# Performance work log

Measured on AMD Instinct MI355X. Metric: run time of the kernel, lower is better.

Reference implementation:

```python
import jax, jax.numpy as jnp
import numpy as np

B, S, H = 2, 2048, 2048
NH, NG = 16, 4           # attention heads, query groups
HD = H // NH             # head_dim = 128
HPG = NH // NG           # heads per group = 4


def setup_inputs() -> dict:
    key = jax.random.key(0)
    ks = jax.random.split(key, 8)
    s = 0.02
    return {
        "hidden_states": jax.random.normal(ks[0], (B, S, H), dtype=jnp.float32),
        "attention_mask": jnp.ones((B, S), dtype=jnp.int32),
        "Wq": jax.random.normal(ks[1], (H, H), dtype=jnp.float32) * s,
        "bq": jnp.zeros((H,), dtype=jnp.float32),
        "Wk": jax.random.normal(ks[2], (HD * NG, H), dtype=jnp.float32) * s,
        "bk": jnp.zeros((HD * NG,), dtype=jnp.float32),
        "Wv": jax.random.normal(ks[3], (HD * NG, H), dtype=jnp.float32) * s,
        "bv": jnp.zeros((HD * NG,), dtype=jnp.float32),
    }


def reference(hidden_states, attention_mask, Wq, bq, Wk, bk, Wv, bv):
    b, s, _ = hidden_states.shape
    scale = 1.0 / np.sqrt(HD).astype(np.float32)
    # projections (torch Linear: x @ W.T + b)
    q = hidden_states @ Wq.T + bq                      # [b,s,H]
    k = hidden_states @ Wk.T + bk                      # [b,s,NG*HD]
    v = hidden_states @ Wv.T + bv
    # q grouped so that repeat_interleave of k/v along heads == broadcast over heads_per_group
    q = q.reshape(b, s, NG, HPG, HD)                   # heads = group-major order
    k = k.reshape(b, s, NG, HD)
    v = v.reshape(b, s, NG, HD)
    scores = jnp.einsum("bsgpd,btgd->bgpst", q, k) * scale  # [b,NG,HPG,s,s]
    # mask: positions with attention_mask == 0 get finfo.min added
    mask_add = jnp.where(attention_mask == 0,
                         jnp.finfo(scores.dtype).min,
                         jnp.float32(0.0))             # [b,t]
    scores = scores + mask_add[:, None, None, None, :]
    attn = jax.nn.softmax(scores, axis=-1)             # dropout is identity in eval
    out = jnp.einsum("bgpst,btgd->bsgpd", attn, v)     # [b,s,NG,HPG,HD]
    return out.reshape(b, s, NH * HD)
```

## Files before the change

### kernel.cpp

```cpp
#include <hip/hip_runtime.h>
#include <hip/hip_bf16.h>

#define B_ 2
#define S_ 2048
#define H_ 2048
#define NH_ 16
#define NG_ 4
#define HD_ 128
#define HPG_ 4

typedef __attribute__((ext_vector_type(8))) short short8;
typedef __attribute__((ext_vector_type(4))) short short4v;
typedef __attribute__((ext_vector_type(4))) float float4v;

#define MFMA_BF16 __builtin_amdgcn_mfma_f32_16x16x32_bf16

#if __has_builtin(__builtin_amdgcn_exp2f)
#define EXP2(x) __builtin_amdgcn_exp2f(x)
#else
#define EXP2(x) exp2f(x)
#endif

__device__ __forceinline__ void gload16(const void* g, void* l) {
    __builtin_amdgcn_global_load_lds(
        (const __attribute__((address_space(1))) unsigned int*)g,
        (__attribute__((address_space(3))) unsigned int*)l, 16, 0, 0);
}

__device__ __forceinline__ short bf16bits(float f) {
    union { __hip_bfloat16 h; short s; } u;
    u.h = __float2bfloat16(f);
    return u.s;
}

__global__ __launch_bounds__(256) void cvt_all(const float* __restrict__ hs,
                                               const float* __restrict__ wq,
                                               const float* __restrict__ wk,
                                               const float* __restrict__ wv,
                                               const int* __restrict__ mask,
                                               const float* __restrict__ bq,
                                               const float* __restrict__ bk,
                                               const float* __restrict__ bv,
                                               __hip_bfloat16* __restrict__ o_hs,
                                               __hip_bfloat16* __restrict__ o_wq,
                                               __hip_bfloat16* __restrict__ o_wk,
                                               __hip_bfloat16* __restrict__ o_wv,
                                               float* __restrict__ o_m,
                                               float* __restrict__ o_bc) {
    int i = blockIdx.x * 256 + threadIdx.x;
    if (blockIdx.x == 0) {
#pragma unroll
        for (int j = 0; j < 16; ++j) {
            int idx = threadIdx.x * 16 + j;
            o_m[idx] = mask[idx] ? 0.0f : -3.0e38f;
        }
    }
    if (blockIdx.x == 1) {
#pragma unroll
        for (int j = 0; j < 12; ++j) {
            int idx = j * 256 + threadIdx.x;
            float v = (idx < 2048) ? bq[idx] : (idx < 2560) ? bk[idx - 2048] : bv[idx - 2560];
            o_bc[idx] = v;
        }
    }
    const float* src;
    __hip_bfloat16* dst;
    int off;
    if (i < 1048576)      { src = hs; dst = o_hs; off = i; }
    else if (i < 1572864) { src = wq; dst = o_wq; off = i - 1048576; }
    else if (i < 1703936) { src = wk; dst = o_wk; off = i - 1572864; }
    else                  { src = wv; dst = o_wv; off = i - 1703936; }
    const float4* s4 = (const float4*)src;
    float4 a = s4[2 * (size_t)off];
    float4 b = s4[2 * (size_t)off + 1];
    union { short8 s; __hip_bfloat16 h[8]; } u;
    u.h[0] = __float2bfloat16(a.x); u.h[1] = __float2bfloat16(a.y);
    u.h[2] = __float2bfloat16(a.z); u.h[3] = __float2bfloat16(a.w);
    u.h[4] = __float2bfloat16(b.x); u.h[5] = __float2bfloat16(b.y);
    u.h[6] = __float2bfloat16(b.z); u.h[7] = __float2bfloat16(b.w);
    *(short8*)(dst + 8 * (size_t)off) = u.s;
}

__global__ __launch_bounds__(512, 2) void gemm_qkv3(const __hip_bfloat16* __restrict__ A,
                                                    const __hip_bfloat16* __restrict__ Wcat,
                                                    const float* __restrict__ biasC,
                                                    __hip_bfloat16* __restrict__ qO,
                                                    __hip_bfloat16* __restrict__ kO,
                                                    __hip_bfloat16* __restrict__ vTO) {
    extern __shared__ char lds[];

    const int tid = threadIdx.x;
    const int lane = tid & 63;
    const int x = lane & 15, g = lane >> 4;
    const int wid = tid >> 6;
    const int wm = wid >> 2, wn = wid & 3;

    const int id0 = blockIdx.x;
    const int id = ((id0 & 7) << 5) | (id0 >> 3);
    const int bn_t = id >> 4, bm_t = id & 15;
    const int bm = bm_t * 256, bn = bn_t * 192;

    const int srow = tid >> 3;
    const int schunk = (tid & 7) ^ (srow & 7);
    const __hip_bfloat16* gA = A + (size_t)(bm + srow) * 2048 + schunk * 8;
    const __hip_bfloat16* gB = Wcat + (size_t)(bn + srow) * 2048 + schunk * 8;

    int aoff[8][2], boff[3][2];
#pragma unroll
    for (int mb = 0; mb < 8; ++mb)
#pragma unroll
        for (int kk = 0; kk < 2; ++kk)
            aoff[mb][kk] = (wm * 128 + mb * 16 + x) * 128 + (((kk * 4 + g) ^ (x & 7)) * 16);
#pragma unroll
    for (int nb = 0; nb < 3; ++nb)
#pragma unroll
        for (int kk = 0; kk < 2; ++kk)
            boff[nb][kk] = 32768 + (wn * 48 + nb * 16 + x) * 128 + (((kk * 4 + g) ^ (x & 7)) * 16);

    float4v acc[8][3];
#pragma unroll
    for (int i = 0; i < 8; ++i)
#pragma unroll
        for (int j = 0; j < 3; ++j) acc[i][j] = (float4v)0.f;

#pragma unroll
    for (int p = 0; p < 4; ++p)
        gload16(gA + (size_t)p * 131072, lds + p * 8192 + tid * 16);
#pragma unroll
    for (int p = 0; p < 3; ++p)
        gload16(gB + (size_t)p * 131072, lds + 32768 + p * 8192 + tid * 16);
    gA += 64; gB += 64;
    asm volatile("s_waitcnt vmcnt(0)" ::: "memory");
    __builtin_amdgcn_s_barrier();

    for (int t = 0; t < 32; ++t) {
        const char* cur = lds + (t & 1) * 57344;
        char* nxt = lds + ((t & 1) ^ 1) * 57344;

        if (t < 31) {
#pragma unroll
            for (int p = 0; p < 4; ++p)
                gload16(gA + (size_t)p * 131072, nxt + p * 8192 + tid * 16);
#pragma unroll
            for (int p = 0; p < 3; ++p)
                gload16(gB + (size_t)p * 131072, nxt + 32768 + p * 8192 + tid * 16);
            gA += 64; gB += 64;
        }

#pragma unroll
        for (int kk = 0; kk < 2; ++kk) {
            short8 af[8], bf[3];
#pragma unroll
            for (int mb = 0; mb < 8; ++mb) af[mb] = *(const short8*)(cur + aoff[mb][kk]);
#pragma unroll
            for (int nb = 0; nb < 3; ++nb) bf[nb] = *(const short8*)(cur + boff[nb][kk]);
            __builtin_amdgcn_s_setprio(1);
#pragma unroll
            for (int mb = 0; mb < 8; ++mb)
#pragma unroll
                for (int nb = 0; nb < 3; ++nb)
                    acc[mb][nb] = MFMA_BF16(af[mb], bf[nb], acc[mb][nb], 0, 0, 0);
            __builtin_amdgcn_s_setprio(0);
        }

        asm volatile("s_waitcnt vmcnt(0)" ::: "memory");
        __builtin_amdgcn_s_barrier();
    }

#pragma unroll
    for (int mb = 0; mb < 8; ++mb) {
#pragma unroll
        for (int nb = 0; nb < 3; ++nb) {
            const int n = bn + wn * 48 + nb * 16 + x;
            const float bsv = biasC[n];
            const int m0 = bm + wm * 128 + mb * 16 + g * 4;
            if (n < 2048) {
#pragma unroll
                for (int r = 0; r < 4; ++r)
                    qO[(size_t)(m0 + r) * 2048 + n] = __float2bfloat16(acc[mb][nb][r] + bsv);
            } else if (n < 2560) {
                const int nk = n - 2048;
#pragma unroll
                for (int r = 0; r < 4; ++r)
                    kO[(size_t)(m0 + r) * 512 + nk] = __float2bfloat16(acc[mb][nb][r] + bsv);
            } else {
                const int nv = n - 2560;
                const int gv = nv >> 7, d = nv & 127;
                const int bb2 = m0 >> 11, s = m0 & 2047;
                short4v pk;
#pragma unroll
                for (int r = 0; r < 4; ++r) pk[r] = bf16bits(acc[mb][nb][r] + bsv);
                *(short4v*)(vTO + ((size_t)(bb2 * NG_ + gv) * HD_ + d) * S_ + s) = pk;
            }
        }
    }
}

__global__ __launch_bounds__(512, 2) void attn(const __hip_bfloat16* __restrict__ q,
                                               const __hip_bfloat16* __restrict__ k,
                                               const __hip_bfloat16* __restrict__ vT,
                                               const float* __restrict__ M,
                                               float* __restrict__ out) {
    extern __shared__ char smem[];
    char* Ks = smem;
    char* Vs = smem + 32768;
    char* Ps = smem + 49152;

    const int tid = threadIdx.x;
    const int lane = tid & 63;
    const int w = tid >> 6;
    const int wm = w >> 2, wn = w & 3;
    const int x = lane & 15, g = lane >> 4;

    const int bid0 = blockIdx.x;
    const int bid = ((bid0 & 7) << 5) | (bid0 >> 3);
    const int qt = bid & 7;
    const int hp = (bid >> 3) & 3;
    const int gi = (bid >> 5) & 3;
    const int b = bid >> 7;
    const int head = gi * HPG_ + hp;
    const int q0 = qt * 256;

    short8 qf[4][4];
#pragma unroll
    for (int nb = 0; nb < 4; ++nb) {
        const int qq = q0 + wn * 64 + nb * 16 + x;
        const __hip_bfloat16* qrow = q + ((size_t)(b * S_ + qq) * NH_ + head) * HD_ + g * 8;
#pragma unroll
        for (int ks = 0; ks < 4; ++ks)
            qf[nb][ks] = *(const short8*)(qrow + ks * 32);
    }

    const int kchunk = (tid & 15) ^ ((tid >> 4) & 15);
    const __hip_bfloat16* kp = k + ((size_t)(b * S_ + (tid >> 4)) * NG_ + gi) * HD_ + kchunk * 8;
    const int vchunk = (tid & 7) ^ ((tid >> 3) & 7);
    const __hip_bfloat16* vp = vT + ((size_t)(b * NG_ + gi) * HD_ + (tid >> 3)) * S_ + vchunk * 8;
    const float* mp = M + b * S_ + wm * 32 + g * 4;

    float4v O[4][4];
#pragma unroll
    for (int i = 0; i < 4; ++i)
#pragma unroll
        for (int j = 0; j < 4; ++j) O[i][j] = (float4v)0.f;
    float l_part[4] = {0.f, 0.f, 0.f, 0.f};

    const float SM = 0.08838834764831845f * 1.4426950408889634f;

    gload16(kp, Ks + tid * 16);
    gload16(kp + 16384, Ks + tid * 16 + 8192);
    kp += 32768;

    for (int it = 0; it < 32; ++it) {
        __syncthreads();
        const int p = it & 1;
        const char* KsC = Ks + p * 16384;

        float4 mv0 = *(const float4*)(mp);
        float4 mv1 = *(const float4*)(mp + 16);
        mp += 64;
        gload16(vp, Vs + tid * 16);
        gload16(vp + 131072, Vs + tid * 16 + 8192);
        vp += 64;
        if (it < 31) {
            char* KsN = Ks + (p ^ 1) * 16384;
            gload16(kp, KsN + tid * 16);
            gload16(kp + 16384, KsN + tid * 16 + 8192);
            kp += 32768;
        }

        float4v sc[2][4];
#pragma unroll
        for (int i = 0; i < 2; ++i)
#pragma unroll
            for (int j = 0; j < 4; ++j) sc[i][j] = (float4v)0.f;
        __builtin_amdgcn_s_setprio(1);
#pragma unroll
        for (int ks = 0; ks < 4; ++ks) {
            short8 af0 = *(const short8*)(KsC + (wm * 32 + x) * 256 + (((ks * 4 + g) ^ x) * 16));
            short8 af1 = *(const short8*)(KsC + (wm * 32 + 16 + x) * 256 + (((ks * 4 + g) ^ x) * 16));
#pragma unroll
            for (int nb = 0; nb < 4; ++nb) {
                sc[0][nb] = MFMA_BF16(af0, qf[nb][ks], sc[0][nb], 0, 0, 0);
                sc[1][nb] = MFMA_BF16(af1, qf[nb][ks], sc[1][nb], 0, 0, 0);
            }
        }
        __builtin_amdgcn_s_setprio(0);

#pragma unroll
        for (int mb = 0; mb < 2; ++mb) {
            const float4 mv = mb ? mv1 : mv0;
            const int hs = wm * 8 + mb * 4 + g;
#pragma unroll
            for (int nb = 0; nb < 4; ++nb) {
                float p0 = EXP2(fmaf(sc[mb][nb][0], SM, mv.x));
                float p1 = EXP2(fmaf(sc[mb][nb][1], SM, mv.y));
                float p2 = EXP2(fmaf(sc[mb][nb][2], SM, mv.z));
                float p3 = EXP2(fmaf(sc[mb][nb][3], SM, mv.w));
                l_part[nb] += (p0 + p1) + (p2 + p3);
                short4v pk;
                pk[0] = bf16bits(p0); pk[1] = bf16bits(p1);
                pk[2] = bf16bits(p2); pk[3] = bf16bits(p3);
                *(short4v*)(Ps + (wn * 64 + nb * 16 + x) * 136 + hs * 8) = pk;
            }
        }

        __syncthreads();

#pragma unroll
        for (int ks = 0; ks < 2; ++ks) {
            short8 vf[4], pf[4];
#pragma unroll
            for (int i4 = 0; i4 < 4; ++i4) {
                vf[i4] = *(const short8*)(Vs + (wm * 64 + i4 * 16 + x) * 128 +
                                          (((ks * 4 + g) ^ (x & 7)) * 16));
                const char* pb = Ps + (wn * 64 + i4 * 16 + x) * 136 + (8 * ks + 2 * g) * 8;
                union { short4v h[2]; short8 s8; } uu;
                uu.h[0] = *(const short4v*)pb;
                uu.h[1] = *(const short4v*)(pb + 8);
                pf[i4] = uu.s8;
            }
            __builtin_amdgcn_s_setprio(1);
#pragma unroll
            for (int mb = 0; mb < 4; ++mb)
#pragma unroll
                for (int nb = 0; nb < 4; ++nb)
                    O[mb][nb] = MFMA_BF16(vf[mb], pf[nb], O[mb][nb], 0, 0, 0);
            __builtin_amdgcn_s_setprio(0);
        }
    }

    __syncthreads();
#pragma unroll
    for (int nb = 0; nb < 4; ++nb) {
        l_part[nb] += __shfl_xor(l_part[nb], 16);
        l_part[nb] += __shfl_xor(l_part[nb], 32);
    }
    float* lws = (float*)Ps;
    if (g == 0) {
#pragma unroll
        for (int nb = 0; nb < 4; ++nb)
            lws[wm * 256 + wn * 64 + nb * 16 + x] = l_part[nb];
    }
    __syncthreads();
    float inv[4];
#pragma unroll
    for (int nb = 0; nb < 4; ++nb)
        inv[nb] = 1.0f / (l_part[nb] + lws[(wm ^ 1) * 256 + wn * 64 + nb * 16 + x]);

#pragma unroll
    for (int mb = 0; mb < 4; ++mb) {
#pragma unroll
        for (int nb = 0; nb < 4; ++nb) {
            const int qq = q0 + wn * 64 + nb * 16 + x;
            const int d0 = wm * 64 + mb * 16 + g * 4;
            float4v o = O[mb][nb] * inv[nb];
            *(float4v*)(out + (size_t)(b * S_ + qq) * H_ + head * HD_ + d0) = o;
        }
    }
}

extern "C" void kernel_launch(void* const* d_in, const int* in_sizes, int n_in,
                              void* d_out, int out_size, void* d_ws, size_t ws_size,
                              hipStream_t stream) {
    (void)in_sizes; (void)n_in; (void)out_size; (void)ws_size;
    const float* hs = (const float*)d_in[0];
    const int* amask = (const int*)d_in[1];
    const float* Wq = (const float*)d_in[2];
    const float* bq = (const float*)d_in[3];
    const float* Wk = (const float*)d_in[4];
    const float* bk = (const float*)d_in[5];
    const float* Wv = (const float*)d_in[6];
    const float* bv = (const float*)d_in[7];
    float* out = (float*)d_out;

    char* ws = (char*)d_ws;
    __hip_bfloat16* hsB = (__hip_bfloat16*)(ws);
    __hip_bfloat16* WqB = (__hip_bfloat16*)(ws + 16777216);
    __hip_bfloat16* WkB = (__hip_bfloat16*)(ws + 25165824);
    __hip_bfloat16* WvB = (__hip_bfloat16*)(ws + 27262976);
    __hip_bfloat16* qB  = (__hip_bfloat16*)(ws + 29360128);
    __hip_bfloat16* kB  = (__hip_bfloat16*)(ws + 46137344);
    __hip_bfloat16* vTB = (__hip_bfloat16*)(ws + 50331648);
    float* Mf           = (float*)(ws + 54525952);
    float* biasC        = (float*)(ws + 54542336);

    hipFuncSetAttribute((const void*)gemm_qkv3,
                        hipFuncAttributeMaxDynamicSharedMemorySize, 114688);
    hipFuncSetAttribute((const void*)attn,
                        hipFuncAttributeMaxDynamicSharedMemorySize, 83968);

    cvt_all<<<7168, 256, 0, stream>>>(hs, Wq, Wk, Wv, amask, bq, bk, bv,
                                      hsB, WqB, WkB, WvB, Mf, biasC);
    gemm_qkv3<<<256, 512, 114688, stream>>>(hsB, WqB, biasC, qB, kB, vTB);
    attn<<<256, 512, 83968, stream>>>(qB, kB, vTB, Mf, out);
}
```

Measured before the change: 227.0 us.

## Rewrite QKV GEMM with 256x256 tiles and a phased, interleaved load/MFMA pipeline

The QKV projection GEMM moves from 256x192 tiles (256 blocks) to 256x256 tiles (192 blocks) with 128KB LDS and one block per CU. The main loop is split into four sub-phases per K-step, each guarded by barriers and priority bumps, and each issues part of the next tile's global-to-LDS loads while MFMAs run on fragments already in registers. Partial vmcnt waits keep loads in flight across phases. The aim is better data reuse per block and finer overlap of memory with compute, at the cost of lower occupancy and more barriers.

```diff
diff --git a/kernel.cpp b/kernel.cpp
--- a/kernel.cpp
+++ b/kernel.cpp
@@ -81,7 +81,7 @@
     *(short8*)(dst + 8 * (size_t)off) = u.s;
 }
 
-__global__ __launch_bounds__(512, 2) void gemm_qkv3(const __hip_bfloat16* __restrict__ A,
+__global__ __launch_bounds__(512, 1) void gemm_qkv3(const __hip_bfloat16* __restrict__ A,
                                                     const __hip_bfloat16* __restrict__ Wcat,
                                                     const float* __restrict__ biasC,
                                                     __hip_bfloat16* __restrict__ qO,
@@ -96,82 +96,158 @@
     const int wm = wid >> 2, wn = wid & 3;
 
     const int id0 = blockIdx.x;
-    const int id = ((id0 & 7) << 5) | (id0 >> 3);
-    const int bn_t = id >> 4, bm_t = id & 15;
-    const int bm = bm_t * 256, bn = bn_t * 192;
-
-    const int srow = tid >> 3;
-    const int schunk = (tid & 7) ^ (srow & 7);
-    const __hip_bfloat16* gA = A + (size_t)(bm + srow) * 2048 + schunk * 8;
-    const __hip_bfloat16* gB = Wcat + (size_t)(bn + srow) * 2048 + schunk * 8;
-
-    int aoff[8][2], boff[3][2];
+    const int id = (id0 & 7) * 24 + (id0 >> 3);
+    const int bn_t = id / 16, bm_t = id % 16;
+    const int bm = bm_t * 256, bn = bn_t * 256;
+
+    const int row0 = tid >> 3;
+    const int sch = (tid & 7) ^ (row0 & 7);
+
+    char* b0 = lds;
+    char* b1 = lds + 65536;
+
+    auto stA = [&](int t, int h, char* reg) {
+        const __hip_bfloat16* s = A + (size_t)(bm + h * 128 + row0) * 2048 + t * 64 + sch * 8;
+        gload16(s, reg + tid * 16);
+        gload16(s + (size_t)64 * 2048, reg + 8192 + tid * 16);
+    };
+    auto stB = [&](int t, int h, char* reg) {
+        const __hip_bfloat16* s = Wcat + (size_t)(bn + h * 128 + row0) * 2048 + t * 64 + sch * 8;
+        gload16(s, reg + tid * 16);
+        gload16(s + (size_t)64 * 2048, reg + 8192 + tid * 16);
+    };
+
+    int aoff[8][2], boff[4][2];
 #pragma unroll
     for (int mb = 0; mb < 8; ++mb)
 #pragma unroll
         for (int kk = 0; kk < 2; ++kk)
-            aoff[mb][kk] = (wm * 128 + mb * 16 + x) * 128 + (((kk * 4 + g) ^ (x & 7)) * 16);
-#pragma unroll
-    for (int nb = 0; nb < 3; ++nb)
-#pragma unroll
-        for (int kk = 0; kk < 2; ++kk)
-            boff[nb][kk] = 32768 + (wn * 48 + nb * 16 + x) * 128 + (((kk * 4 + g) ^ (x & 7)) * 16);
-
-    float4v acc[8][3];
+            aoff[mb][kk] = wm * 16384 + (mb * 16 + x) * 128 + (((kk * 4 + g) ^ (x & 7)) * 16);
+#pragma unroll
+    for (int nb = 0; nb < 4; ++nb)
+#pragma unroll
+        for (int kk = 0; kk < 2; ++kk) {
+            const int row = wn * 64 + nb * 16 + x;
+            boff[nb][kk] = 32768 + (row >> 7) * 16384 + (row & 127) * 128 +
+                           (((kk * 4 + g) ^ (x & 7)) * 16);
+        }
+
+    float4v acc[8][4];
 #pragma unroll
     for (int i = 0; i < 8; ++i)
 #pragma unroll
-        for (int j = 0; j < 3; ++j) acc[i][j] = (float4v)0.f;
-
-#pragma unroll
-    for (int p = 0; p < 4; ++p)
-        gload16(gA + (size_t)p * 131072, lds + p * 8192 + tid * 16);
-#pragma unroll
-    for (int p = 0; p < 3; ++p)
-        gload16(gB + (size_t)p * 131072, lds + 32768 + p * 8192 + tid * 16);
-    gA += 64; gB += 64;
-    asm volatile("s_waitcnt vmcnt(0)" ::: "memory");
+        for (int j = 0; j < 4; ++j) acc[i][j] = (float4v)0.f;
+
+    stA(0, 0, b0);           stA(0, 1, b0 + 16384);
+    stB(0, 0, b0 + 32768);   stB(0, 1, b0 + 49152);
+    stB(1, 0, b1 + 32768);   stB(1, 1, b1 + 49152);
+    asm volatile("s_waitcnt vmcnt(4)" ::: "memory");
     __builtin_amdgcn_s_barrier();
 
-    for (int t = 0; t < 32; ++t) {
-        const char* cur = lds + (t & 1) * 57344;
-        char* nxt = lds + ((t & 1) ^ 1) * 57344;
-
-        if (t < 31) {
-#pragma unroll
-            for (int p = 0; p < 4; ++p)
-                gload16(gA + (size_t)p * 131072, nxt + p * 8192 + tid * 16);
-#pragma unroll
-            for (int p = 0; p < 3; ++p)
-                gload16(gB + (size_t)p * 131072, nxt + 32768 + p * 8192 + tid * 16);
-            gA += 64; gB += 64;
-        }
-
-#pragma unroll
-        for (int kk = 0; kk < 2; ++kk) {
-            short8 af[8], bf[3];
-#pragma unroll
-            for (int mb = 0; mb < 8; ++mb) af[mb] = *(const short8*)(cur + aoff[mb][kk]);
-#pragma unroll
-            for (int nb = 0; nb < 3; ++nb) bf[nb] = *(const short8*)(cur + boff[nb][kk]);
-            __builtin_amdgcn_s_setprio(1);
-#pragma unroll
-            for (int mb = 0; mb < 8; ++mb)
-#pragma unroll
-                for (int nb = 0; nb < 3; ++nb)
-                    acc[mb][nb] = MFMA_BF16(af[mb], bf[nb], acc[mb][nb], 0, 0, 0);
-            __builtin_amdgcn_s_setprio(0);
-        }
-
-        asm volatile("s_waitcnt vmcnt(0)" ::: "memory");
+    short8 af[4][2], bf[4][2];
+
+#define PH_SYNC()                                   \
+    __builtin_amdgcn_s_barrier();                   \
+    asm volatile("s_waitcnt lgkmcnt(0)");           \
+    __builtin_amdgcn_sched_barrier(0);              \
+    __builtin_amdgcn_s_setprio(1)
+
+#define PH_END()                                    \
+    __builtin_amdgcn_s_setprio(0);                  \
+    __builtin_amdgcn_s_barrier()
+
+#define MFMA_Q(MB0, NB0)                            \
+    _Pragma("unroll")                               \
+    for (int mb = 0; mb < 4; ++mb)                  \
+        _Pragma("unroll")                           \
+        for (int nb = 0; nb < 2; ++nb)              \
+            _Pragma("unroll")                       \
+            for (int kk = 0; kk < 2; ++kk)          \
+                acc[MB0 + mb][NB0 + nb] =           \
+                    MFMA_BF16(af[mb][kk], bf[NB0 + nb][kk], acc[MB0 + mb][NB0 + nb], 0, 0, 0)
+
+    for (int i = 0; i < 16; ++i) {
+        const int t1 = 2 * i + 1;
+#pragma unroll
+        for (int mb = 0; mb < 4; ++mb)
+#pragma unroll
+            for (int kk = 0; kk < 2; ++kk) af[mb][kk] = *(const short8*)(b0 + aoff[mb][kk]);
+#pragma unroll
+        for (int nb = 0; nb < 2; ++nb)
+#pragma unroll
+            for (int kk = 0; kk < 2; ++kk) bf[nb][kk] = *(const short8*)(b0 + boff[nb][kk]);
+        stA(t1, 0, b1);
+        PH_SYNC(); MFMA_Q(0, 0); PH_END();
+
+#pragma unroll
+        for (int nb = 2; nb < 4; ++nb)
+#pragma unroll
+            for (int kk = 0; kk < 2; ++kk) bf[nb][kk] = *(const short8*)(b0 + boff[nb][kk]);
+        stA(t1, 1, b1 + 16384);
+        PH_SYNC(); MFMA_Q(0, 2); PH_END();
+
+#pragma unroll
+        for (int mb = 0; mb < 4; ++mb)
+#pragma unroll
+            for (int kk = 0; kk < 2; ++kk) af[mb][kk] = *(const short8*)(b0 + aoff[4 + mb][kk]);
+        if (i < 15) stB(2 * i + 2, 0, b0 + 32768);
+        PH_SYNC(); MFMA_Q(4, 0); PH_END();
+
+        if (i < 15) stB(2 * i + 2, 1, b0 + 49152);
         __builtin_amdgcn_s_barrier();
-    }
+        asm volatile("s_waitcnt lgkmcnt(0)");
+        __builtin_amdgcn_sched_barrier(0);
+        __builtin_amdgcn_s_setprio(1);
+        MFMA_Q(4, 2);
+        __builtin_amdgcn_s_setprio(0);
+        if (i < 15) asm volatile("s_waitcnt vmcnt(4)" ::: "memory");
+        else        asm volatile("s_waitcnt vmcnt(0)" ::: "memory");
+        __builtin_amdgcn_s_barrier();
+
+#pragma unroll
+        for (int mb = 0; mb < 4; ++mb)
+#pragma unroll
+            for (int kk = 0; kk < 2; ++kk) af[mb][kk] = *(const short8*)(b1 + aoff[mb][kk]);
+#pragma unroll
+        for (int nb = 0; nb < 2; ++nb)
+#pragma unroll
+            for (int kk = 0; kk < 2; ++kk) bf[nb][kk] = *(const short8*)(b1 + boff[nb][kk]);
+        if (i < 15) stA(2 * i + 2, 0, b0);
+        PH_SYNC(); MFMA_Q(0, 0); PH_END();
+
+#pragma unroll
+        for (int nb = 2; nb < 4; ++nb)
+#pragma unroll
+            for (int kk = 0; kk < 2; ++kk) bf[nb][kk] = *(const short8*)(b1 + boff[nb][kk]);
+        if (i < 15) stA(2 * i + 2, 1, b0 + 16384);
+        PH_SYNC(); MFMA_Q(0, 2); PH_END();
+
+#pragma unroll
+        for (int mb = 0; mb < 4; ++mb)
+#pragma unroll
+            for (int kk = 0; kk < 2; ++kk) af[mb][kk] = *(const short8*)(b1 + aoff[4 + mb][kk]);
+        if (i < 15) stB(2 * i + 3, 0, b1 + 32768);
+        PH_SYNC(); MFMA_Q(4, 0); PH_END();
+
+        if (i < 15) stB(2 * i + 3, 1, b1 + 49152);
+        __builtin_amdgcn_s_barrier();
+        asm volatile("s_waitcnt lgkmcnt(0)");
+        __builtin_amdgcn_sched_barrier(0);
+        __builtin_amdgcn_s_setprio(1);
+        MFMA_Q(4, 2);
+        __builtin_amdgcn_s_setprio(0);
+        if (i < 15) asm volatile("s_waitcnt vmcnt(4)" ::: "memory");
+        __builtin_amdgcn_s_barrier();
+    }
+#undef PH_SYNC
+#undef PH_END
+#undef MFMA_Q
 
 #pragma unroll
     for (int mb = 0; mb < 8; ++mb) {
 #pragma unroll
-        for (int nb = 0; nb < 3; ++nb) {
-            const int n = bn + wn * 48 + nb * 16 + x;
+        for (int nb = 0; nb < 4; ++nb) {
+            const int n = bn + wn * 64 + nb * 16 + x;
             const float bsv = biasC[n];
             const int m0 = bm + wm * 128 + mb * 16 + g * 4;
             if (n < 2048) {
@@ -385,12 +461,12 @@
     float* biasC        = (float*)(ws + 54542336);
 
     hipFuncSetAttribute((const void*)gemm_qkv3,
-                        hipFuncAttributeMaxDynamicSharedMemorySize, 114688);
+                        hipFuncAttributeMaxDynamicSharedMemorySize, 131072);
     hipFuncSetAttribute((const void*)attn,
                         hipFuncAttributeMaxDynamicSharedMemorySize, 83968);
 
     cvt_all<<<7168, 256, 0, stream>>>(hs, Wq, Wk, Wv, amask, bq, bk, bv,
                                       hsB, WqB, WkB, WvB, Mf, biasC);
-    gemm_qkv3<<<256, 512, 114688, stream>>>(hsB, WqB, biasC, qB, kB, vTB);
+    gemm_qkv3<<<192, 512, 131072, stream>>>(hsB, WqB, biasC, qB, kB, vTB);
     attn<<<256, 512, 83968, stream>>>(qB, kB, vTB, Mf, out);
 }
```

New measurement: 279.3 us. 1.23x slower.
